# Optimization experiments

Hardware: AMD Instinct MI355X
Metric: run time of the kernel (lower is better)

Reference implementation:

```python
import jax, jax.numpy as jnp
import numpy as np

B, CIN, COUT, T, J = 64, 128, 128, 128, 25
EPS = 1e-5  # BatchNorm2d default eps


def setup_inputs() -> dict:
    key = jax.random.key(0)
    k = jax.random.split(key, 5)
    x = jax.random.normal(k[0], (B, CIN, T, J), jnp.float32)
    adj = jax.random.normal(k[1], (J, J), jnp.float32) / np.sqrt(J).astype(np.float32)
    Wk = jax.random.normal(k[2], (COUT, CIN), jnp.float32) / np.sqrt(CIN).astype(np.float32)
    Wq = jax.random.normal(k[3], (COUT, CIN), jnp.float32) / np.sqrt(CIN).astype(np.float32)
    Ws = jax.random.normal(k[4], (COUT, CIN), jnp.float32) / np.sqrt(CIN).astype(np.float32)
    return {
        "x": x, "adj": adj,
        "Wk": Wk, "bk": jnp.zeros((COUT,), jnp.float32),
        "Wq": Wq, "bq": jnp.zeros((COUT,), jnp.float32),
        "Ws": Ws, "bs": jnp.zeros((COUT,), jnp.float32),
        "gamma": jnp.ones((COUT,), jnp.float32),
        "beta": jnp.zeros((COUT,), jnp.float32),
        "run_mean": jnp.zeros((COUT,), jnp.float32),
        "run_var": jnp.ones((COUT,), jnp.float32),
        "alpha": jnp.ones((1,), jnp.float32),
    }


def reference(x, adj, Wk, bk, Wq, bq, Ws, bs, gamma, beta, run_mean, run_var, alpha):
    # static graph conv: aggregate over joints with the shared adjacency
    static = jnp.einsum('bctj,jk->bctk', x, adj)              # [B,Cin,T,J]
    # 1x1 conv == channel matmul
    static_feat = jnp.einsum('oc,bctj->botj', Ws, static) + bs[None, :, None, None]  # [B,Cout,T,J]
    # temporal mean pooling, then key/query 1x1 convs
    x_t = x.mean(axis=2)                                      # [B,Cin,J]
    kk = jnp.einsum('oc,bcj->boj', Wk, x_t) + bk[None, :, None]  # [B,Cout,J]
    qq = jnp.einsum('oc,bcj->boj', Wq, x_t) + bq[None, :, None]  # [B,Cout,J]
    # attention-style dynamic adjacency: softmax(q^T k / sqrt(Cout)) over last axis
    scale = jnp.sqrt(jnp.asarray(kk.shape[1], x.dtype))
    scores = jnp.einsum('bcj,bck->bjk', qq, kk) / scale       # [B,J,J]
    dyn = jax.nn.softmax(scores, axis=-1)                     # [B,J,J]
    # original expands dyn to (B*T, Cout, J, J); same math without materialization:
    dyn_feat = jnp.einsum('bctj,bjk->bctk', static_feat, dyn)  # [B,Cout,T,J]
    out = static_feat + alpha[0] * dyn_feat
    # BatchNorm2d in inference mode (running stats), then ReLU
    inv = gamma[None, :, None, None] * jax.lax.rsqrt(run_var[None, :, None, None] + EPS)
    out = (out - run_mean[None, :, None, None]) * inv + beta[None, :, None, None]
    return jax.nn.relu(out)
```

## Files before the change

### kernel.cpp

```cpp
#include <hip/hip_runtime.h>

#define B_ 64
#define C_ 128
#define T_ 128
#define J_ 25
#define PIT 136
#define XP 40
#define GP 136
#define TT 4

typedef unsigned short ushort_t;
typedef __attribute__((ext_vector_type(8))) unsigned short ushort8;
typedef __attribute__((ext_vector_type(4))) unsigned short ushort4_t;
typedef __attribute__((ext_vector_type(8))) _Float16 half8;
typedef __attribute__((ext_vector_type(4))) float f32x4;
typedef float f32x4u __attribute__((ext_vector_type(4), aligned(4)));
typedef unsigned short ushort8u __attribute__((ext_vector_type(8), aligned(2)));

__device__ __forceinline__ float bf2f(ushort_t u) {
  unsigned int v = ((unsigned int)u) << 16;
  return __builtin_bit_cast(float, v);
}
__device__ __forceinline__ ushort_t f2bf(float f) {
  unsigned int u = __builtin_bit_cast(unsigned int, f);
  u += 0x7FFFu + ((u >> 16) & 1u);
  return (ushort_t)(u >> 16);
}
__device__ __forceinline__ ushort_t f2h_bits(float f) {
  _Float16 h = (_Float16)f;
  return __builtin_bit_cast(ushort_t, h);
}
__device__ __forceinline__ float h2f(ushort_t u) {
  return (float)__builtin_bit_cast(_Float16, u);
}
__device__ __forceinline__ half8 cvt_bf8_h8(ushort8 u) {
  half8 r;
#pragma unroll
  for (int i = 0; i < 8; ++i) r[i] = (_Float16)bf2f(u[i]);
  return r;
}
__device__ __forceinline__ float ldv(const void* p, long i, int isf32) {
  return isf32 ? ((const float*)p)[i] : bf2f(((const ushort_t*)p)[i]);
}
__device__ __forceinline__ half8 ld8h(const void* p, long i, int isf32) {
  half8 r;
  if (isf32) {
    const float* f = (const float*)p + i;
#pragma unroll
    for (int k = 0; k < 8; ++k) r[k] = (_Float16)f[k];
  } else {
    ushort8 u = *(const ushort8*)((const ushort_t*)p + i);
    r = cvt_bf8_h8(u);
  }
  return r;
}

__device__ __forceinline__ int detect_isf32(const void* p, int tid) {
  const ushort_t* u = (const ushort_t*)p;
  float a = fabsf(bf2f(u[2 * (tid & 63)]));
  int ok = (a > 1e-4f && a < 64.f) ? 1 : 0;
  unsigned long long m = __ballot(ok);
  return (__popcll(m) > 32) ? 0 : 1;
}

__global__ __launch_bounds__(256) void k_mean(const void* __restrict__ x,
                                              float* __restrict__ xt) {
  const int bc = blockIdx.x;
  const int b = bc >> 7, c = bc & 127;
  const long base = (long)bc * 3200;
  const int tid = threadIdx.x;
  const int isf32 = detect_isf32((const ushort_t*)x + base, tid);
  __shared__ float pl[3200];
  __shared__ float red[8][32];
  if (isf32) {
    const f32x4* src = (const f32x4*)((const float*)x + base);
    for (int i = tid; i < 800; i += 256) *(f32x4*)&pl[i * 4] = src[i];
  } else {
    const ushort4_t* src = (const ushort4_t*)((const ushort_t*)x + base);
    for (int i = tid; i < 800; i += 256) {
      ushort4_t u = src[i];
      f32x4 v;
#pragma unroll
      for (int r = 0; r < 4; ++r) v[r] = bf2f(u[r]);
      *(f32x4*)&pl[i * 4] = v;
    }
  }
  __syncthreads();
  const int j = tid & 31, g = tid >> 5;
  float s = 0.f;
  if (j < J_) {
#pragma unroll
    for (int i = 0; i < 16; ++i) s += pl[(g * 16 + i) * 25 + j];
  }
  red[g][j] = s;
  __syncthreads();
  if (tid < 32) {
    float tot = 0.f;
#pragma unroll
    for (int gg = 0; gg < 8; ++gg) tot += red[gg][tid];
    if (tid < J_) xt[b * 4096 + tid * 128 + c] = tot * (1.0f / 128.0f);
  }
}

__global__ __launch_bounds__(256) void k_attn(
    const float* __restrict__ xt, const void* __restrict__ adj,
    const void* __restrict__ Wk, const void* __restrict__ bk,
    const void* __restrict__ Wq, const void* __restrict__ bq,
    const void* __restrict__ alphap, ushort_t* __restrict__ fkws,
    float* __restrict__ sws) {
  const int b = blockIdx.x;
  const int tid = threadIdx.x;
  const int isf32 = detect_isf32(Wk, tid);
  const int wv = tid >> 6, lane = tid & 63, lrow = lane & 15, quad = lane >> 4;
  const float alpha = ldv(alphap, 0, isf32);

  __shared__ __align__(16) ushort_t xtT[32 * PIT];
  __shared__ __align__(16) ushort_t kkT[32 * PIT];
  __shared__ __align__(16) ushort_t qqT[32 * PIT];
  __shared__ float sc[32 * 33];

  for (int idx = tid; idx < 32 * PIT; idx += 256) {
    int r = idx / PIT, col = idx % PIT;
    float v = (r < J_ && col < 128) ? xt[b * 4096 + r * 128 + col] : 0.f;
    xtT[idx] = f2h_bits(v);
  }
  __syncthreads();

  for (int mat = 0; mat < 2; ++mat) {
    const void* W = mat ? Wq : Wk;
    const void* bias = mat ? bq : bk;
    ushort_t* dstT = mat ? qqT : kkT;
    f32x4 acc[2][2] = {};
    for (int ks = 0; ks < 4; ++ks) {
      half8 bfr[2];
#pragma unroll
      for (int jt = 0; jt < 2; ++jt)
        bfr[jt] = *(const half8*)&xtT[(jt * 16 + lrow) * PIT + ks * 32 + quad * 8];
#pragma unroll
      for (int ot = 0; ot < 2; ++ot) {
        int o = (2 * wv + ot) * 16 + lrow;
        half8 afr = ld8h(W, o * 128 + ks * 32 + quad * 8, isf32);
#pragma unroll
        for (int jt = 0; jt < 2; ++jt)
          acc[ot][jt] = __builtin_amdgcn_mfma_f32_16x16x32_f16(afr, bfr[jt],
                                                               acc[ot][jt], 0, 0, 0);
      }
    }
#pragma unroll
    for (int ot = 0; ot < 2; ++ot) {
      int obase = (2 * wv + ot) * 16 + quad * 4;
#pragma unroll
      for (int jt = 0; jt < 2; ++jt) {
        int j = jt * 16 + lrow;
        ushort_t pack[4];
#pragma unroll
        for (int r = 0; r < 4; ++r)
          pack[r] = f2h_bits(acc[ot][jt][r] + ldv(bias, obase + r, isf32));
        *(ushort4_t*)&dstT[j * PIT + obase] = *(ushort4_t*)pack;
      }
    }
  }
  __syncthreads();

  {
    const int mt = wv >> 1, nt = wv & 1;
    f32x4 acc = {};
    for (int ks = 0; ks < 4; ++ks) {
      half8 afr = *(const half8*)&qqT[(mt * 16 + lrow) * PIT + ks * 32 + quad * 8];
      half8 bfr = *(const half8*)&kkT[(nt * 16 + lrow) * PIT + ks * 32 + quad * 8];
      acc = __builtin_amdgcn_mfma_f32_16x16x32_f16(afr, bfr, acc, 0, 0, 0);
    }
    const float rs = 0.08838834764831845f;
#pragma unroll
    for (int r = 0; r < 4; ++r)
      sc[(mt * 16 + quad * 4 + r) * 33 + nt * 16 + lrow] = acc[r] * rs;
  }
  __syncthreads();

  if (tid < J_) {
    float m = -1e30f;
    for (int k = 0; k < J_; ++k) m = fmaxf(m, sc[tid * 33 + k]);
    float sum = 0.f;
    for (int k = 0; k < J_; ++k) {
      float e = expf(sc[tid * 33 + k] - m);
      sc[tid * 33 + k] = e;
      sum += e;
    }
    float inv = 1.f / sum;
    for (int k = 0; k < J_; ++k) sc[tid * 33 + k] *= inv;
  }
  __syncthreads();

  for (int idx = tid; idx < 1280; idx += 256) {
    int k = idx / XP, jj = idx % XP;
    float v = 0.f;
    if (k < J_ && jj < J_) {
      v = ldv(adj, jj * J_ + k, isf32);
      float d = 0.f;
      for (int m = 0; m < J_; ++m) d += ldv(adj, jj * J_ + m, isf32) * sc[m * 33 + k];
      v += alpha * d;
    }
    fkws[b * 1280 + idx] = f2h_bits(v);
  }
  if (tid < 32) {
    float v = 0.f;
    if (tid < J_) {
      float d = 0.f;
      for (int jj = 0; jj < J_; ++jj) d += sc[jj * 33 + tid];
      v = 1.f + alpha * d;
    }
    sws[b * 32 + tid] = v;
  }
}

#define SM_FK 0
#define SM_GT 2560
#define SM_TOT 33024
__global__ __launch_bounds__(256, 4) void k_main(
    const void* __restrict__ x, const void* __restrict__ Ws,
    const void* __restrict__ bs, const void* __restrict__ gamma,
    const void* __restrict__ beta, const void* __restrict__ rmean,
    const void* __restrict__ rvar, const ushort_t* __restrict__ fkws,
    const float* __restrict__ sws, void* __restrict__ out) {
  const int tid = threadIdx.x;
  const int isf32 = detect_isf32(Ws, tid);
  const int b = blockIdx.x >> 5, tb = blockIdx.x & 31, t0 = tb * TT;
  const int wv = tid >> 6, lane = tid & 63, lrow = lane & 15, quad = lane >> 4;

  __shared__ __align__(16) char smem[SM_TOT];
  __shared__ float bnscale[128], bnshift[128], bsv[128], sv[32];
  ushort_t* fk = (ushort_t*)(smem + SM_FK);
  ushort_t* gt = (ushort_t*)(smem + SM_GT);
  ushort_t* outbuf = (ushort_t*)(smem + SM_GT);

  half8 wsf[2][4];
#pragma unroll
  for (int ot = 0; ot < 2; ++ot) {
    int o = (2 * wv + ot) * 16 + lrow;
#pragma unroll
    for (int ks = 0; ks < 4; ++ks)
      wsf[ot][ks] = ld8h(Ws, o * 128 + ks * 32 + quad * 8, isf32);
  }

  for (int i = tid; i < 160; i += 256)
    *(ushort8*)&fk[i * 8] = *(const ushort8*)&fkws[b * 1280 + i * 8];
  for (int i = tid; i < 204; i += 256) {
    int row = 100 + i / 17, col8 = (i % 17) * 8;
    ushort8 z = {};
    *(ushort8*)&gt[row * GP + col8] = z;
  }
  if (tid < 32) sv[tid] = sws[b * 32 + tid];
  if (tid < 128) {
    float g = ldv(gamma, tid, isf32), v = ldv(rvar, tid, isf32);
    float scl = g * rsqrtf(v + 1e-5f);
    bnscale[tid] = scl;
    bnshift[tid] = ldv(beta, tid, isf32) - ldv(rmean, tid, isf32) * scl;
    bsv[tid] = ldv(bs, tid, isf32);
  }
  __syncthreads();

  {
    half8 afr[2];
#pragma unroll
    for (int mt = 0; mt < 2; ++mt)
      afr[mt] = *(const half8*)&fk[(mt * 16 + lrow) * XP + quad * 8];
    const float* xf = (const float*)x;
    const ushort_t* xh = (const ushort_t*)x;
#pragma unroll
    for (int t = 0; t < TT; ++t) {
#pragma unroll
      for (int ci = 0; ci < 2; ++ci) {
        int ct = 2 * wv + ci;
        long p = (long)b * 409600 + (long)(ct * 16 + lrow) * 3200 + (t0 + t) * 25;
        half8 bfr;
        if (quad < 3) {
          if (isf32) {
            f32x4u v0 = *(const f32x4u*)(xf + p + quad * 8);
            f32x4u v1 = *(const f32x4u*)(xf + p + quad * 8 + 4);
#pragma unroll
            for (int r = 0; r < 4; ++r) {
              bfr[r] = (_Float16)v0[r];
              bfr[4 + r] = (_Float16)v1[r];
            }
          } else {
            ushort8u u = *(const ushort8u*)(xh + p + quad * 8);
#pragma unroll
            for (int r = 0; r < 8; ++r) bfr[r] = (_Float16)bf2f(u[r]);
          }
        } else {
          bfr = (half8){};
          bfr[0] = (_Float16)(isf32 ? xf[p + 24] : bf2f(xh[p + 24]));
        }
        f32x4 accg[2] = {};
#pragma unroll
        for (int mt = 0; mt < 2; ++mt)
          accg[mt] = __builtin_amdgcn_mfma_f32_16x16x32_f16(afr[mt], bfr, accg[mt], 0, 0, 0);
#pragma unroll
        for (int mt = 0; mt < 2; ++mt)
#pragma unroll
          for (int r = 0; r < 4; ++r) {
            int kk = mt * 16 + quad * 4 + r;
            if (kk < J_)
              gt[(t * 25 + kk) * GP + ct * 16 + lrow] = f2h_bits(accg[mt][r]);
          }
      }
    }
  }
  __syncthreads();

  f32x4 acc[2][7];
#pragma unroll
  for (int ot = 0; ot < 2; ++ot)
#pragma unroll
    for (int nt = 0; nt < 7; ++nt) acc[ot][nt] = (f32x4){};
  for (int ks = 0; ks < 4; ++ks) {
#pragma unroll
    for (int nt = 0; nt < 7; ++nt) {
      half8 bfr = *(const half8*)&gt[(nt * 16 + lrow) * GP + ks * 32 + quad * 8];
#pragma unroll
      for (int ot = 0; ot < 2; ++ot)
        acc[ot][nt] = __builtin_amdgcn_mfma_f32_16x16x32_f16(wsf[ot][ks], bfr,
                                                             acc[ot][nt], 0, 0, 0);
    }
  }
  __syncthreads();

#pragma unroll
  for (int nt = 0; nt < 7; ++nt) {
    int n = nt * 16 + lrow;
    if (n < 100) {
      float svk = sv[n % 25];
#pragma unroll
      for (int ot = 0; ot < 2; ++ot) {
        int obase = (2 * wv + ot) * 16 + quad * 4;
#pragma unroll
        for (int r = 0; r < 4; ++r) {
          int o = obase + r;
          float v = acc[ot][nt][r] + bsv[o] * svk;
          v = v * bnscale[o] + bnshift[o];
          outbuf[o * 100 + n] = f2h_bits(fmaxf(v, 0.f));
        }
      }
    }
  }
  __syncthreads();

  {
    const long obase = ((long)(b * 128) * 128 + t0) * 25;
    if (isf32) {
      float* of = (float*)out + obase;
      for (int idx = tid; idx < 3200; idx += 256) {
        int o = idx / 25, q = idx % 25;
        ushort4_t u = *(const ushort4_t*)&outbuf[o * 100 + q * 4];
        f32x4 v;
#pragma unroll
        for (int r = 0; r < 4; ++r) v[r] = h2f(u[r]);
        *(f32x4*)(of + (long)o * 3200 + q * 4) = v;
      }
    } else {
      ushort_t* oh = (ushort_t*)out + obase;
      for (int idx = tid; idx < 3200; idx += 256) {
        int o = idx / 25, q = idx % 25;
        ushort4_t u = *(const ushort4_t*)&outbuf[o * 100 + q * 4];
        ushort4_t w;
#pragma unroll
        for (int r = 0; r < 4; ++r) w[r] = f2bf(h2f(u[r]));
        *(ushort4_t*)(oh + (long)o * 3200 + q * 4) = w;
      }
    }
  }
}

extern "C" void kernel_launch(void* const* d_in, const int* in_sizes, int n_in,
                              void* d_out, int out_size, void* d_ws, size_t ws_size,
                              hipStream_t stream) {
  const void* x = d_in[0];
  const void* adj = d_in[1];
  const void* Wk = d_in[2];
  const void* bk = d_in[3];
  const void* Wq = d_in[4];
  const void* bq = d_in[5];
  const void* Ws = d_in[6];
  const void* bsp = d_in[7];
  const void* gamma = d_in[8];
  const void* beta = d_in[9];
  const void* rmean = d_in[10];
  const void* rvar = d_in[11];
  const void* alphap = d_in[12];

  char* ws = (char*)d_ws;
  float* xt = (float*)ws;
  ushort_t* fkws = (ushort_t*)(ws + 64 * 4096 * 4);
  float* sws = (float*)(ws + 64 * 4096 * 4 + 64 * 1280 * 2);

  k_mean<<<B_ * C_, 256, 0, stream>>>(x, xt);
  k_attn<<<B_, 256, 0, stream>>>(xt, adj, Wk, bk, Wq, bq, alphap, fkws, sws);
  k_main<<<B_ * (T_ / TT), 256, 0, stream>>>(x, Ws, bsp, gamma, beta, rmean, rvar,
                                             fkws, sws, d_out);
}
```

Measured before the change: 300.0 us.

## Vectorize loads, store mean as fp16, parallelize attention, prefetch x in main kernel

Several independent tweaks land together. The Wk/Wq loads and the bf16 mean loads become wider vector loads, and the temporal mean is stored as fp16 so k_attn can copy it with 16-byte loads. k_attn now uses 512 threads so the key and query projections run concurrently, and it caches the adjacency matrix in shared memory. k_main prefetches its x tiles into registers before the setup phase, shrinks shared memory by dropping the zero-padded rows, masks their loads instead, and raises the occupancy hint to 5 blocks. The costs are more register pressure in k_main and an fp16 round of the mean, though that value was already converted to fp16 before the MFMA.

```diff
diff --git a/kernel.cpp b/kernel.cpp
--- a/kernel.cpp
+++ b/kernel.cpp
@@ -46,8 +46,13 @@
   half8 r;
   if (isf32) {
     const float* f = (const float*)p + i;
-#pragma unroll
-    for (int k = 0; k < 8; ++k) r[k] = (_Float16)f[k];
+    f32x4 v0 = *(const f32x4*)f;
+    f32x4 v1 = *(const f32x4*)(f + 4);
+#pragma unroll
+    for (int k = 0; k < 4; ++k) {
+      r[k] = (_Float16)v0[k];
+      r[4 + k] = (_Float16)v1[k];
+    }
   } else {
     ushort8 u = *(const ushort8*)((const ushort_t*)p + i);
     r = cvt_bf8_h8(u);
@@ -64,7 +69,7 @@
 }
 
 __global__ __launch_bounds__(256) void k_mean(const void* __restrict__ x,
-                                              float* __restrict__ xt) {
+                                              ushort_t* __restrict__ xt) {
   const int bc = blockIdx.x;
   const int b = bc >> 7, c = bc & 127;
   const long base = (long)bc * 3200;
@@ -76,13 +81,17 @@
     const f32x4* src = (const f32x4*)((const float*)x + base);
     for (int i = tid; i < 800; i += 256) *(f32x4*)&pl[i * 4] = src[i];
   } else {
-    const ushort4_t* src = (const ushort4_t*)((const ushort_t*)x + base);
-    for (int i = tid; i < 800; i += 256) {
-      ushort4_t u = src[i];
-      f32x4 v;
-#pragma unroll
-      for (int r = 0; r < 4; ++r) v[r] = bf2f(u[r]);
-      *(f32x4*)&pl[i * 4] = v;
+    const ushort8* src = (const ushort8*)((const ushort_t*)x + base);
+    for (int i = tid; i < 400; i += 256) {
+      ushort8 u = src[i];
+      f32x4 v0, v1;
+#pragma unroll
+      for (int r = 0; r < 4; ++r) {
+        v0[r] = bf2f(u[r]);
+        v1[r] = bf2f(u[4 + r]);
+      }
+      *(f32x4*)&pl[i * 8] = v0;
+      *(f32x4*)&pl[i * 8 + 4] = v1;
     }
   }
   __syncthreads();
@@ -98,12 +107,12 @@
     float tot = 0.f;
 #pragma unroll
     for (int gg = 0; gg < 8; ++gg) tot += red[gg][tid];
-    if (tid < J_) xt[b * 4096 + tid * 128 + c] = tot * (1.0f / 128.0f);
-  }
-}
-
-__global__ __launch_bounds__(256) void k_attn(
-    const float* __restrict__ xt, const void* __restrict__ adj,
+    if (tid < J_) xt[b * 4096 + tid * 128 + c] = f2h_bits(tot * (1.0f / 128.0f));
+  }
+}
+
+__global__ __launch_bounds__(512) void k_attn(
+    const ushort_t* __restrict__ xt, const void* __restrict__ adj,
     const void* __restrict__ Wk, const void* __restrict__ bk,
     const void* __restrict__ Wq, const void* __restrict__ bq,
     const void* __restrict__ alphap, ushort_t* __restrict__ fkws,
@@ -112,24 +121,29 @@
   const int tid = threadIdx.x;
   const int isf32 = detect_isf32(Wk, tid);
   const int wv = tid >> 6, lane = tid & 63, lrow = lane & 15, quad = lane >> 4;
+  const int mg = wv >> 2, wvv = wv & 3;
   const float alpha = ldv(alphap, 0, isf32);
 
   __shared__ __align__(16) ushort_t xtT[32 * PIT];
   __shared__ __align__(16) ushort_t kkT[32 * PIT];
   __shared__ __align__(16) ushort_t qqT[32 * PIT];
   __shared__ float sc[32 * 33];
-
-  for (int idx = tid; idx < 32 * PIT; idx += 256) {
-    int r = idx / PIT, col = idx % PIT;
-    float v = (r < J_ && col < 128) ? xt[b * 4096 + r * 128 + col] : 0.f;
-    xtT[idx] = f2h_bits(v);
-  }
-  __syncthreads();
-
-  for (int mat = 0; mat < 2; ++mat) {
-    const void* W = mat ? Wq : Wk;
-    const void* bias = mat ? bq : bk;
-    ushort_t* dstT = mat ? qqT : kkT;
+  __shared__ float adjL[25 * 26];
+
+  for (int idx = tid; idx < 32 * 17; idx += 512) {
+    int r = idx / 17, c8 = idx % 17;
+    ushort8 v = {};
+    if (r < J_ && c8 < 16) v = *(const ushort8*)&xt[b * 4096 + r * 128 + c8 * 8];
+    *(ushort8*)&xtT[r * PIT + c8 * 8] = v;
+  }
+  for (int idx = tid; idx < 625; idx += 512)
+    adjL[(idx / 25) * 26 + (idx % 25)] = ldv(adj, idx, isf32);
+  __syncthreads();
+
+  {
+    const void* W = mg ? Wq : Wk;
+    const void* bias = mg ? bq : bk;
+    ushort_t* dstT = mg ? qqT : kkT;
     f32x4 acc[2][2] = {};
     for (int ks = 0; ks < 4; ++ks) {
       half8 bfr[2];
@@ -138,7 +152,7 @@
         bfr[jt] = *(const half8*)&xtT[(jt * 16 + lrow) * PIT + ks * 32 + quad * 8];
 #pragma unroll
       for (int ot = 0; ot < 2; ++ot) {
-        int o = (2 * wv + ot) * 16 + lrow;
+        int o = (2 * wvv + ot) * 16 + lrow;
         half8 afr = ld8h(W, o * 128 + ks * 32 + quad * 8, isf32);
 #pragma unroll
         for (int jt = 0; jt < 2; ++jt)
@@ -148,7 +162,7 @@
     }
 #pragma unroll
     for (int ot = 0; ot < 2; ++ot) {
-      int obase = (2 * wv + ot) * 16 + quad * 4;
+      int obase = (2 * wvv + ot) * 16 + quad * 4;
 #pragma unroll
       for (int jt = 0; jt < 2; ++jt) {
         int j = jt * 16 + lrow;
@@ -162,7 +176,7 @@
   }
   __syncthreads();
 
-  {
+  if (wv < 4) {
     const int mt = wv >> 1, nt = wv & 1;
     f32x4 acc = {};
     for (int ks = 0; ks < 4; ++ks) {
@@ -191,13 +205,13 @@
   }
   __syncthreads();
 
-  for (int idx = tid; idx < 1280; idx += 256) {
+  for (int idx = tid; idx < 1280; idx += 512) {
     int k = idx / XP, jj = idx % XP;
     float v = 0.f;
     if (k < J_ && jj < J_) {
-      v = ldv(adj, jj * J_ + k, isf32);
+      v = adjL[jj * 26 + k];
       float d = 0.f;
-      for (int m = 0; m < J_; ++m) d += ldv(adj, jj * J_ + m, isf32) * sc[m * 33 + k];
+      for (int m = 0; m < J_; ++m) d += adjL[jj * 26 + m] * sc[m * 33 + k];
       v += alpha * d;
     }
     fkws[b * 1280 + idx] = f2h_bits(v);
@@ -215,8 +229,8 @@
 
 #define SM_FK 0
 #define SM_GT 2560
-#define SM_TOT 33024
-__global__ __launch_bounds__(256, 4) void k_main(
+#define SM_TOT (2560 + 100 * GP * 2)
+__global__ __launch_bounds__(256, 5) void k_main(
     const void* __restrict__ x, const void* __restrict__ Ws,
     const void* __restrict__ bs, const void* __restrict__ gamma,
     const void* __restrict__ beta, const void* __restrict__ rmean,
@@ -233,6 +247,39 @@
   ushort_t* gt = (ushort_t*)(smem + SM_GT);
   ushort_t* outbuf = (ushort_t*)(smem + SM_GT);
 
+  half8 xa[TT][2];
+  {
+    const float* xf = (const float*)x;
+    const ushort_t* xh = (const ushort_t*)x;
+#pragma unroll
+    for (int t = 0; t < TT; ++t)
+#pragma unroll
+      for (int ci = 0; ci < 2; ++ci) {
+        const int ct = 2 * wv + ci;
+        const long p = (long)b * 409600 + (long)(ct * 16 + lrow) * 3200 + (t0 + t) * 25;
+        half8 bfr;
+        if (quad < 3) {
+          if (isf32) {
+            f32x4u v0 = *(const f32x4u*)(xf + p + quad * 8);
+            f32x4u v1 = *(const f32x4u*)(xf + p + quad * 8 + 4);
+#pragma unroll
+            for (int r = 0; r < 4; ++r) {
+              bfr[r] = (_Float16)v0[r];
+              bfr[4 + r] = (_Float16)v1[r];
+            }
+          } else {
+            ushort8u u = *(const ushort8u*)(xh + p + quad * 8);
+#pragma unroll
+            for (int r = 0; r < 8; ++r) bfr[r] = (_Float16)bf2f(u[r]);
+          }
+        } else {
+          bfr = (half8){};
+          bfr[0] = (_Float16)(isf32 ? xf[p + 24] : bf2f(xh[p + 24]));
+        }
+        xa[t][ci] = bfr;
+      }
+  }
+
   half8 wsf[2][4];
 #pragma unroll
   for (int ot = 0; ot < 2; ++ot) {
@@ -244,11 +291,6 @@
 
   for (int i = tid; i < 160; i += 256)
     *(ushort8*)&fk[i * 8] = *(const ushort8*)&fkws[b * 1280 + i * 8];
-  for (int i = tid; i < 204; i += 256) {
-    int row = 100 + i / 17, col8 = (i % 17) * 8;
-    ushort8 z = {};
-    *(ushort8*)&gt[row * GP + col8] = z;
-  }
   if (tid < 32) sv[tid] = sws[b * 32 + tid];
   if (tid < 128) {
     float g = ldv(gamma, tid, isf32), v = ldv(rvar, tid, isf32);
@@ -264,42 +306,21 @@
 #pragma unroll
     for (int mt = 0; mt < 2; ++mt)
       afr[mt] = *(const half8*)&fk[(mt * 16 + lrow) * XP + quad * 8];
-    const float* xf = (const float*)x;
-    const ushort_t* xh = (const ushort_t*)x;
 #pragma unroll
     for (int t = 0; t < TT; ++t) {
 #pragma unroll
       for (int ci = 0; ci < 2; ++ci) {
-        int ct = 2 * wv + ci;
-        long p = (long)b * 409600 + (long)(ct * 16 + lrow) * 3200 + (t0 + t) * 25;
-        half8 bfr;
-        if (quad < 3) {
-          if (isf32) {
-            f32x4u v0 = *(const f32x4u*)(xf + p + quad * 8);
-            f32x4u v1 = *(const f32x4u*)(xf + p + quad * 8 + 4);
-#pragma unroll
-            for (int r = 0; r < 4; ++r) {
-              bfr[r] = (_Float16)v0[r];
-              bfr[4 + r] = (_Float16)v1[r];
-            }
-          } else {
-            ushort8u u = *(const ushort8u*)(xh + p + quad * 8);
-#pragma unroll
-            for (int r = 0; r < 8; ++r) bfr[r] = (_Float16)bf2f(u[r]);
-          }
-        } else {
-          bfr = (half8){};
-          bfr[0] = (_Float16)(isf32 ? xf[p + 24] : bf2f(xh[p + 24]));
-        }
+        const int ct = 2 * wv + ci;
         f32x4 accg[2] = {};
 #pragma unroll
         for (int mt = 0; mt < 2; ++mt)
-          accg[mt] = __builtin_amdgcn_mfma_f32_16x16x32_f16(afr[mt], bfr, accg[mt], 0, 0, 0);
+          accg[mt] = __builtin_amdgcn_mfma_f32_16x16x32_f16(afr[mt], xa[t][ci],
+                                                            accg[mt], 0, 0, 0);
 #pragma unroll
         for (int mt = 0; mt < 2; ++mt)
 #pragma unroll
           for (int r = 0; r < 4; ++r) {
-            int kk = mt * 16 + quad * 4 + r;
+            const int kk = mt * 16 + quad * 4 + r;
             if (kk < J_)
               gt[(t * 25 + kk) * GP + ct * 16 + lrow] = f2h_bits(accg[mt][r]);
           }
@@ -316,7 +337,9 @@
   for (int ks = 0; ks < 4; ++ks) {
 #pragma unroll
     for (int nt = 0; nt < 7; ++nt) {
-      half8 bfr = *(const half8*)&gt[(nt * 16 + lrow) * GP + ks * 32 + quad * 8];
+      half8 bfr = (half8){};
+      if (nt < 6 || lrow < 4)
+        bfr = *(const half8*)&gt[(nt * 16 + lrow) * GP + ks * 32 + quad * 8];
 #pragma unroll
       for (int ot = 0; ot < 2; ++ot)
         acc[ot][nt] = __builtin_amdgcn_mfma_f32_16x16x32_f16(wsf[ot][ks], bfr,
@@ -389,12 +412,12 @@
   const void* alphap = d_in[12];
 
   char* ws = (char*)d_ws;
-  float* xt = (float*)ws;
-  ushort_t* fkws = (ushort_t*)(ws + 64 * 4096 * 4);
-  float* sws = (float*)(ws + 64 * 4096 * 4 + 64 * 1280 * 2);
+  ushort_t* xt = (ushort_t*)ws;
+  ushort_t* fkws = (ushort_t*)(ws + 64 * 4096 * 2);
+  float* sws = (float*)(ws + 64 * 4096 * 2 + 64 * 1280 * 2);
 
   k_mean<<<B_ * C_, 256, 0, stream>>>(x, xt);
-  k_attn<<<B_, 256, 0, stream>>>(xt, adj, Wk, bk, Wq, bq, alphap, fkws, sws);
+  k_attn<<<B_, 512, 0, stream>>>(xt, adj, Wk, bk, Wq, bq, alphap, fkws, sws);
   k_main<<<B_ * (T_ / TT), 256, 0, stream>>>(x, Ws, bsp, gamma, beta, rmean, rvar,
                                              fkws, sws, d_out);
 }
```

After: 311.2 us. +3.8%, slower.
